# Performance work log

Measured on AMD Instinct MI355X. Metric: run time of the kernel, lower is better.

Reference implementation:

```python
import jax, jax.numpy as jnp
import numpy as np

LN_EPS = 1e-5

def _dw_conv_dilated(h, w, dil):
    # replicate-pad then VALID dilated depthwise 3x3 conv (groups = channels)
    hp = jnp.pad(h, ((0, 0), (0, 0), (dil, dil), (dil, dil)), mode='edge')
    return jax.lax.conv_general_dilated(
        hp, w, window_strides=(1, 1), padding='VALID', rhs_dilation=(dil, dil),
        dimension_numbers=('NCHW', 'OIHW', 'NCHW'), feature_group_count=h.shape[1])

def setup_inputs() -> dict:
    key = jax.random.key(0)
    ks = jax.random.split(key, 16)
    B, l, d_model = 4, 4096, 512
    d_inner, d_state, dt_rank = 512, 1, 32
    return {
        'x': jax.random.normal(ks[0], (B, l, d_model), jnp.float32),
        'in_proj_w': jax.random.normal(ks[1], (2 * d_inner, d_model), jnp.float32) * 0.02,
        'conv2d_w': jax.random.normal(ks[2], (d_inner, 1, 3, 3), jnp.float32) * 0.1,
        'conv2d_b': jax.random.normal(ks[3], (d_inner,), jnp.float32) * 0.1,
        'x_proj_weight': jax.random.normal(ks[4], (dt_rank + 2 * d_state, d_inner), jnp.float32) * 0.02,
        'dt_projs_weight': jax.random.normal(ks[5], (d_inner, dt_rank), jnp.float32) * 0.1,
        'dt_projs_bias': jax.random.normal(ks[6], (d_inner,), jnp.float32) * 0.1,
        'A_logs': jax.random.normal(ks[7], (d_inner, d_state), jnp.float32),
        'Ds': jax.random.normal(ks[8], (d_inner,), jnp.float32),
        'sf_k3': jax.random.normal(ks[9], (d_inner, 1, 3, 3), jnp.float32) * 0.1,
        'sf_k3_1': jax.random.normal(ks[10], (d_inner, 1, 3, 3), jnp.float32) * 0.1,
        'sf_k3_2': jax.random.normal(ks[11], (d_inner, 1, 3, 3), jnp.float32) * 0.1,
        'sf_alpha': jax.random.normal(ks[12], (3,), jnp.float32),
        'ln_w': jnp.ones((d_inner,), jnp.float32),
        'ln_b': jnp.zeros((d_inner,), jnp.float32),
        'out_proj_w': jax.random.normal(ks[13], (d_model, d_inner), jnp.float32) * 0.02,
    }

def reference(x, in_proj_w, conv2d_w, conv2d_b, x_proj_weight, dt_projs_weight,
              dt_projs_bias, A_logs, Ds, sf_k3, sf_k3_1, sf_k3_2, sf_alpha,
              ln_w, ln_b, out_proj_w):
    B, l, C = x.shape
    sqrt_l = int(np.ceil(np.sqrt(l)))
    new_l = sqrt_l * sqrt_l
    xp = jnp.pad(x, ((0, 0), (0, new_l - l), (0, 0)))
    xg = xp.reshape(B, sqrt_l, sqrt_l, C)                  # b h w c
    xz = xg @ in_proj_w.T                                  # b h w 2d
    d_inner = in_proj_w.shape[0] // 2
    xin, z = xz[..., :d_inner], xz[..., d_inner:]
    xc = jnp.transpose(xin, (0, 3, 1, 2))                  # b d h w
    xc = jax.lax.conv_general_dilated(
        xc, conv2d_w, (1, 1), 'SAME',
        dimension_numbers=('NCHW', 'OIHW', 'NCHW'),
        feature_group_count=d_inner) + conv2d_b[None, :, None, None]
    xc = jax.nn.silu(xc)
    H = W = sqrt_l
    L = H * W
    xs = xc.reshape(B, d_inner, L)                         # b d l
    x_dbl = jnp.einsum('kd,bdl->bkl', x_proj_weight, xs)
    R = dt_projs_weight.shape[1]
    N = A_logs.shape[1]                                    # == 1
    dts = jnp.einsum('dr,brl->bdl', dt_projs_weight, x_dbl[:, :R])
    Bs = x_dbl[:, R:R + N]                                 # b n l
    Cs = x_dbl[:, R + N:R + 2 * N]                         # b n l
    A = -jnp.exp(A_logs)                                   # d n
    delta = jax.nn.softplus(dts + dt_projs_bias[None, :, None])  # b d l
    # selective scan via associative scan: h_t = a_t * h_{t-1} + b_t
    a = jnp.exp(delta[:, :, None, :] * A[None, :, :, None])       # b d n l
    bb = delta[:, :, None, :] * Bs[:, None, :, :] * xs[:, :, None, :]
    def combine(c1, c2):
        a1, b1 = c1
        a2, b2 = c2
        return (a1 * a2, a2 * b1 + b2)
    _, h = jax.lax.associative_scan(combine, (a, bb), axis=-1)
    h = h[:, :, 0, :].reshape(B, d_inner, H, W)            # n == 1
    # StateFusion: 3 dilated replicate-padded depthwise convs
    h = (sf_alpha[0] * _dw_conv_dilated(h, sf_k3, 1)
         + sf_alpha[1] * _dw_conv_dilated(h, sf_k3_1, 2)
         + sf_alpha[2] * _dw_conv_dilated(h, sf_k3_2, 3))
    h = h.reshape(B, d_inner, L)
    y = h * Cs + xs * Ds[None, :, None]                    # Cs (b,1,l) broadcasts
    y = jnp.transpose(y, (0, 2, 1))                        # b l d
    mu = jnp.mean(y, axis=-1, keepdims=True)
    var = jnp.var(y, axis=-1, keepdims=True)
    y = (y - mu) / jnp.sqrt(var + LN_EPS) * ln_w + ln_b
    y = y * jax.nn.silu(z.reshape(B, L, d_inner))
    y = y @ out_proj_w.T
    return y[:, :l, :]
```

## Files before the change

kernel.cpp:

```cpp
#include <hip/hip_runtime.h>
#include <cstddef>


typedef __attribute__((ext_vector_type(8))) short short8;
typedef __attribute__((ext_vector_type(8))) unsigned short ushort8_t;
typedef __attribute__((ext_vector_type(4))) float f32x4;

__device__ __forceinline__ void gload16(const void* g, void* l) {
  __builtin_amdgcn_global_load_lds(
      (const __attribute__((address_space(1))) void*)g,
      (__attribute__((address_space(3))) void*)l, 16, 0, 0);
}

__device__ __forceinline__ void bf16split(float v, unsigned short& h, unsigned short& l) {
  unsigned u = __float_as_uint(v);
  unsigned uh = (u + 0x7fffu + ((u >> 16) & 1u)) & 0xffff0000u;
  h = (unsigned short)(uh >> 16);
  float rem = v - __uint_as_float(uh);
  unsigned ur = __float_as_uint(rem);
  l = (unsigned short)((ur + 0x7fffu + ((ur >> 16) & 1u)) >> 16);
}

__device__ __forceinline__ unsigned short bf16rne(float v) {
  unsigned u = __float_as_uint(v);
  return (unsigned short)((u + 0x7fffu + ((u >> 16) & 1u)) >> 16);
}

__device__ __forceinline__ float b2f(unsigned short u) {
  return __uint_as_float((unsigned)u << 16);
}

__global__ __launch_bounds__(256)
void split_k(const float* __restrict__ in, unsigned short* __restrict__ hi,
             unsigned short* __restrict__ lo, int n4)
{
  int i = blockIdx.x * 256 + threadIdx.x;
  if (i >= n4) return;
  float4 v = ((const float4*)in)[i];
  float vv[4] = {v.x, v.y, v.z, v.w};
  unsigned short h[4], l[4];
#pragma unroll
  for (int j = 0; j < 4; ++j) bf16split(vv[j], h[j], l[j]);
  ((ushort4*)hi)[i] = make_ushort4(h[0], h[1], h[2], h[3]);
  ((ushort4*)lo)[i] = make_ushort4(l[0], l[1], l[2], l[3]);
}

__global__ __launch_bounds__(256)
void cvt_hi_k(const float* __restrict__ in, unsigned short* __restrict__ hi, int n4)
{
  int i = blockIdx.x * 256 + threadIdx.x;
  if (i >= n4) return;
  float4 v = ((const float4*)in)[i];
  ((ushort4*)hi)[i] = make_ushort4(bf16rne(v.x), bf16rne(v.y), bf16rne(v.z), bf16rne(v.w));
}

__global__ __launch_bounds__(256, 2)
void gemm0_k(const unsigned short* __restrict__ Ahi, const unsigned short* __restrict__ Whi,
             const unsigned short* __restrict__ Wlo,
             unsigned short* __restrict__ xinb, unsigned short* __restrict__ zb16)
{
  __shared__ char smem[65536];
  unsigned short* sA  = (unsigned short*)smem;
  unsigned short* sBh = (unsigned short*)(smem + 32768);
  unsigned short* sBl = (unsigned short*)(smem + 49152);
  const int tid = threadIdx.x;
  const int wave = tid >> 6, lane = tid & 63;

  const int nwg = gridDim.x;
  const int q = nwg >> 3, r = nwg & 7;
  const int xcd = blockIdx.x & 7, wi = blockIdx.x >> 3;
  const int logical = (xcd < r ? xcd * (q + 1) : r * (q + 1) + (xcd - r) * q) + wi;
  const int tm = logical >> 3, tn = logical & 7;
  const int m0 = tm << 8;
  const int n0 = tn << 7;
  const bool two = (n0 < 512);

  const int wm = (wave & 1) << 7;
  const int wn = (wave >> 1) << 6;
  const int q16 = (lane >> 4) << 4;
  const int l15 = lane & 15;

  int srA[8], scA[8];
#pragma unroll
  for (int c = 0; c < 8; ++c) {
    int o = (wave << 13) + (c << 10) + (lane << 4);
    int row = o >> 7;
    srA[c] = row;
    scA[c] = (o & 127) ^ ((row & 7) << 4);
  }
  int srB[4], scB[4];
#pragma unroll
  for (int c = 0; c < 4; ++c) {
    int o = (wave << 12) + (c << 10) + (lane << 4);
    int row = o >> 7;
    srB[c] = row;
    scB[c] = (o & 127) ^ ((row & 7) << 4);
  }

  f32x4 acc[8][4];
#pragma unroll
  for (int i = 0; i < 8; ++i)
#pragma unroll
    for (int j = 0; j < 4; ++j) acc[i][j] = (f32x4){0.f, 0.f, 0.f, 0.f};

  for (int kt = 0; kt < 8; ++kt) {
    int kb = kt << 7;
    __syncthreads();
#pragma unroll
    for (int c = 0; c < 8; ++c)
      gload16((const char*)Ahi + (size_t)(m0 + srA[c]) * 1024 + kb + scA[c],
              (char*)sA + (wave << 13) + (c << 10));
#pragma unroll
    for (int c = 0; c < 4; ++c) {
      size_t gb = (size_t)(n0 + srB[c]) * 1024 + kb + scB[c];
      int lo_ = (wave << 12) + (c << 10);
      gload16((const char*)Whi + gb, (char*)sBh + lo_);
      if (two) gload16((const char*)Wlo + gb, (char*)sBl + lo_);
    }
    __syncthreads();
#pragma unroll
    for (int ks = 0; ks < 2; ++ks) {
      short8 af[8], bh[4], bl[4];
#pragma unroll
      for (int i = 0; i < 8; ++i) {
        int row = wm + (i << 4) + l15;
        int cb = ((ks << 6) + q16) ^ ((row & 7) << 4);
        af[i] = *(const short8*)((const char*)sA + (row << 7) + cb);
      }
#pragma unroll
      for (int j = 0; j < 4; ++j) {
        int row = wn + (j << 4) + l15;
        int cb = ((ks << 6) + q16) ^ ((row & 7) << 4);
        bh[j] = *(const short8*)((const char*)sBh + (row << 7) + cb);
        if (two) bl[j] = *(const short8*)((const char*)sBl + (row << 7) + cb);
      }
#pragma unroll
      for (int i = 0; i < 8; ++i)
#pragma unroll
        for (int j = 0; j < 4; ++j) {
          acc[i][j] = __builtin_amdgcn_mfma_f32_16x16x32_bf16(af[i], bh[j], acc[i][j], 0, 0, 0);
          if (two)
            acc[i][j] = __builtin_amdgcn_mfma_f32_16x16x32_bf16(af[i], bl[j], acc[i][j], 0, 0, 0);
        }
    }
  }

  const int mb_base = m0 + wm + ((lane >> 4) << 2);
#pragma unroll
  for (int j = 0; j < 4; ++j) {
    int n = n0 + wn + (j << 4) + l15;
#pragma unroll
    for (int i = 0; i < 8; ++i) {
      int mb = mb_base + (i << 4);
      if (n < 512) {
        int b = mb >> 12, l = mb & 4095;
        ushort4 hv = make_ushort4(bf16rne(acc[i][j][0]), bf16rne(acc[i][j][1]),
                                  bf16rne(acc[i][j][2]), bf16rne(acc[i][j][3]));
        *(ushort4*)&xinb[((size_t)(b * 512 + n) << 12) + l] = hv;
      } else {
#pragma unroll
        for (int rr = 0; rr < 4; ++rr)
          zb16[(size_t)(mb + rr) * 512 + (n - 512)] = bf16rne(acc[i][j][rr]);
      }
    }
  }
}

__global__ __launch_bounds__(256)
void gemm1_k(const unsigned short* __restrict__ Ag_, const unsigned short* __restrict__ Whi,
             float* __restrict__ o1)
{
  __shared__ char smem[32768];
  unsigned short* sA  = (unsigned short*)smem;
  unsigned short* sBh = (unsigned short*)(smem + 16384);
  const int tid = threadIdx.x;
  const int wave = tid >> 6, lane = tid & 63;

  const int nwg = gridDim.x;
  const int q = nwg >> 3, r = nwg & 7;
  const int xcd = blockIdx.x & 7, wi = blockIdx.x >> 3;
  const int logical = (xcd < r ? xcd * (q + 1) : r * (q + 1) + (xcd - r) * q) + wi;
  const int tm = logical >> 2, tn = logical & 3;
  const int m0 = tm << 7, n0 = tn << 7;

  const int wm = (wave & 1) << 6;
  const int wn = (wave >> 1) << 6;
  const int q16 = (lane >> 4) << 4;
  const int l15 = lane & 15;

  int srow[4], scol[4];
#pragma unroll
  for (int c = 0; c < 4; ++c) {
    int o = (wave << 12) + (c << 10) + (lane << 4);
    int row = o >> 7;
    srow[c] = row;
    scol[c] = (o & 127) ^ ((row & 7) << 4);
  }

  f32x4 acc[4][4];
#pragma unroll
  for (int i = 0; i < 4; ++i)
#pragma unroll
    for (int j = 0; j < 4; ++j) acc[i][j] = (f32x4){0.f, 0.f, 0.f, 0.f};

  for (int kt = 0; kt < 8; ++kt) {
    int kb = kt << 7;
    __syncthreads();
#pragma unroll
    for (int c = 0; c < 4; ++c) {
      size_t ga = (size_t)(m0 + srow[c]) * 1024 + kb + scol[c];
      size_t gb = (size_t)(n0 + srow[c]) * 1024 + kb + scol[c];
      int lo_ = (wave << 12) + (c << 10);
      gload16((const char*)Ag_ + ga, (char*)sA + lo_);
      gload16((const char*)Whi + gb, (char*)sBh + lo_);
    }
    __syncthreads();
#pragma unroll
    for (int ks = 0; ks < 2; ++ks) {
      short8 af[4], bh[4];
#pragma unroll
      for (int i = 0; i < 4; ++i) {
        int row = wm + (i << 4) + l15;
        int cb = ((ks << 6) + q16) ^ ((row & 7) << 4);
        af[i] = *(const short8*)((const char*)sA + (row << 7) + cb);
      }
#pragma unroll
      for (int j = 0; j < 4; ++j) {
        int row = wn + (j << 4) + l15;
        int cb = ((ks << 6) + q16) ^ ((row & 7) << 4);
        bh[j] = *(const short8*)((const char*)sBh + (row << 7) + cb);
      }
#pragma unroll
      for (int i = 0; i < 4; ++i)
#pragma unroll
        for (int j = 0; j < 4; ++j)
          acc[i][j] = __builtin_amdgcn_mfma_f32_16x16x32_bf16(af[i], bh[j], acc[i][j], 0, 0, 0);
    }
  }

  float* sC = (float*)smem;
  const int i_base = (lane >> 4) << 2;
#pragma unroll
  for (int half = 0; half < 2; ++half) {
    __syncthreads();
    if ((wave & 1) == half) {
#pragma unroll
      for (int j = 0; j < 4; ++j) {
        int nl = wn + (j << 4) + l15;
#pragma unroll
        for (int i = 0; i < 4; ++i) {
          int mloc = (i << 4) + i_base;
#pragma unroll
          for (int rr = 0; rr < 4; ++rr)
            sC[(mloc + rr) * 128 + nl] = acc[i][j][rr];
        }
      }
    }
    __syncthreads();
    int cx = (tid & 31) << 2;
    int r0 = tid >> 5;
#pragma unroll
    for (int it = 0; it < 8; ++it) {
      int row = r0 + (it << 3);
      *(float4*)&o1[(size_t)(m0 + (half << 6) + row) * 512 + n0 + cx] =
          *(float4*)&sC[row * 128 + cx];
    }
  }
}

__global__ __launch_bounds__(256)
void conv_silu_k(const unsigned short* __restrict__ xin, const float* __restrict__ w,
                 const float* __restrict__ bias, float* __restrict__ xs)
{
  __shared__ float t[64][65];
  int plane = blockIdx.x;
  int d = plane & 511;
  int tid = threadIdx.x;
  const unsigned short* src = xin + (size_t)plane * 4096;
  int l0 = tid << 4, row = tid >> 2, c0 = (tid & 3) << 4;
  ushort8_t v0 = *(const ushort8_t*)&src[l0];
  ushort8_t v1 = *(const ushort8_t*)&src[l0 + 8];
#pragma unroll
  for (int j = 0; j < 8; ++j) {
    t[row][c0 + j]     = b2f(v0[j]);
    t[row][c0 + 8 + j] = b2f(v1[j]);
  }
  float wv[9];
#pragma unroll
  for (int j = 0; j < 9; j++) wv[j] = w[d * 9 + j];
  float bv = bias[d];
  __syncthreads();
  float* dst = xs + (size_t)plane * 4096;
#pragma unroll
  for (int i = 0; i < 16; i++) {
    int idx = tid + i * 256;
    int y = idx >> 6, x = idx & 63;
    float s = bv;
#pragma unroll
    for (int u = 0; u < 3; u++)
#pragma unroll
      for (int v = 0; v < 3; v++) {
        int yy = y + u - 1, xx = x + v - 1;
        if (yy >= 0 && yy < 64 && xx >= 0 && xx < 64)
          s = fmaf(wv[u * 3 + v], t[yy][xx], s);
      }
    dst[idx] = s * (1.f / (1.f + __expf(-s)));
  }
}

__global__ __launch_bounds__(256)
void xdbl_part_k(const float* __restrict__ xs, const float* __restrict__ xpw,
                 float* __restrict__ partial)
{
  __shared__ float sw[34 * 64];
  int tid = threadIdx.x;
  int p  = blockIdx.x * 256 + tid;
  int d0 = blockIdx.y * 64;
  int b = p >> 12, l = p & 4095;
  for (int i = tid; i < 34 * 64; i += 256) {
    int k = i >> 6, dd = i & 63;
    sw[i] = xpw[k * 512 + d0 + dd];
  }
  __syncthreads();
  float acc[34];
#pragma unroll
  for (int k = 0; k < 34; k++) acc[k] = 0.f;
  const float* xp = xs + (size_t)(b * 512 + d0) * 4096 + l;
#pragma unroll 4
  for (int dd = 0; dd < 64; dd++) {
    float v = xp[(size_t)dd * 4096];
#pragma unroll
    for (int k = 0; k < 34; k++) acc[k] = fmaf(sw[k * 64 + dd], v, acc[k]);
  }
  float* op = partial + (size_t)blockIdx.y * 34 * 16384 + p;
#pragma unroll
  for (int k = 0; k < 34; k++) op[(size_t)k * 16384] = acc[k];
}

__global__ __launch_bounds__(256)
void xdbl_reduce_k(const float* __restrict__ partial, float* __restrict__ xdbl_r)
{
  int gid = blockIdx.x * 256 + threadIdx.x;
  float s = 0.f;
#pragma unroll
  for (int sp = 0; sp < 8; sp++) s += partial[(size_t)sp * 34 * 16384 + gid];
  xdbl_r[gid] = s;
}

__global__ __launch_bounds__(256)
void delta_k(const float* __restrict__ xdbl_r, const float* __restrict__ dtw,
             const float* __restrict__ dtb, float* __restrict__ del)
{
  __shared__ float sm[32][256];
  int tid = threadIdx.x;
  int l0 = blockIdx.x * 256;
  int d0 = blockIdx.y * 64;
  int b  = blockIdx.z;
  int p0 = b * 4096 + l0;
#pragma unroll
  for (int k = 0; k < 32; k++) sm[k][tid] = xdbl_r[k * 16384 + p0 + tid];
  __syncthreads();
#pragma unroll 2
  for (int dd = 0; dd < 64; dd++) {
    int d = d0 + dd;
    float s = dtb[d];
#pragma unroll
    for (int r = 0; r < 32; r++) s = fmaf(dtw[d * 32 + r], sm[r][tid], s);
    float delta = fmaxf(s, 0.f) + __logf(1.f + __expf(-fabsf(s)));
    del[((size_t)(b * 512 + d) << 12) + l0 + tid] = delta;
  }
}

__global__ __launch_bounds__(256)
void scan_sfconv_k(const float* __restrict__ del, const float* __restrict__ Bsr,
                   const float* __restrict__ xs, const float* __restrict__ A_logs,
                   const float* __restrict__ k1, const float* __restrict__ k2,
                   const float* __restrict__ k3, const float* __restrict__ alpha,
                   const float* __restrict__ Cs, const float* __restrict__ Ds,
                   unsigned short* __restrict__ ypre)
{
  __shared__ float t[64][65];
  __shared__ float segA[4], segH[4];
  int plane = blockIdx.x;
  int d = plane & 511;
  int b = plane >> 9;
  int tid = threadIdx.x;
  int wave = tid >> 6, lane = tid & 63;
  size_t base = (size_t)plane * 4096;
  float Ad = -__expf(A_logs[d]);

  const int l0 = tid << 4;
  float a_reg[16], b_reg[16], x_reg[16];
#pragma unroll
  for (int k = 0; k < 4; ++k) {
    float4 dv4 = *(const float4*)&del[base + l0 + k * 4];
    float4 bs4 = *(const float4*)&Bsr[(b << 12) + l0 + k * 4];
    float4 xs4 = *(const float4*)&xs[base + l0 + k * 4];
    float dv[4] = {dv4.x, dv4.y, dv4.z, dv4.w};
    float bs[4] = {bs4.x, bs4.y, bs4.z, bs4.w};
    float xv[4] = {xs4.x, xs4.y, xs4.z, xs4.w};
#pragma unroll
    for (int j = 0; j < 4; ++j) {
      a_reg[k * 4 + j] = __expf(dv[j] * Ad);
      b_reg[k * 4 + j] = dv[j] * bs[j] * xv[j];
      x_reg[k * 4 + j] = xv[j];
    }
  }

  float A_th = a_reg[0], H_th = b_reg[0];
#pragma unroll
  for (int j = 1; j < 16; ++j) {
    H_th = fmaf(a_reg[j], H_th, b_reg[j]);
    A_th *= a_reg[j];
  }

#pragma unroll
  for (int off = 1; off < 64; off <<= 1) {
    float Ap = __shfl_up(A_th, off);
    float Hp = __shfl_up(H_th, off);
    if (lane >= off) { H_th = fmaf(A_th, Hp, H_th); A_th *= Ap; }
  }
  float eA = __shfl_up(A_th, 1);
  float eH = __shfl_up(H_th, 1);
  if (lane == 0) { eA = 1.f; eH = 0.f; }
  if (lane == 63) { segA[wave] = A_th; segH[wave] = H_th; }
  __syncthreads();

  float cy1 = segH[0];
  float cy2 = fmaf(segA[1], cy1, segH[1]);
  float cy3 = fmaf(segA[2], cy2, segH[2]);
  float myc = (wave == 1) ? cy1 : (wave == 2) ? cy2 : (wave == 3) ? cy3 : 0.f;
  float h = fmaf(eA, myc, eH);

  int row = tid >> 2, c0 = (tid & 3) << 4;
#pragma unroll
  for (int j = 0; j < 16; ++j) {
    h = fmaf(a_reg[j], h, b_reg[j]);
    t[row][c0 + j] = h;
  }
  __syncthreads();

  float wv[3][9];
  float a0 = alpha[0], a1 = alpha[1], a2 = alpha[2];
#pragma unroll
  for (int j = 0; j < 9; j++) {
    wv[0][j] = a0 * k1[d * 9 + j];
    wv[1][j] = a1 * k2[d * 9 + j];
    wv[2][j] = a2 * k3[d * 9 + j];
  }
  float Dv = Ds[d];
  float cs_reg[16];
#pragma unroll
  for (int k = 0; k < 4; ++k) {
    float4 c4 = *(const float4*)&Cs[(b << 12) + l0 + k * 4];
    cs_reg[k * 4 + 0] = c4.x; cs_reg[k * 4 + 1] = c4.y;
    cs_reg[k * 4 + 2] = c4.z; cs_reg[k * 4 + 3] = c4.w;
  }
  unsigned short ov[16];
  const int y = row;
#pragma unroll
  for (int j = 0; j < 16; j++) {
    int x = c0 + j;
    float s = 0.f;
#pragma unroll
    for (int dil = 1; dil <= 3; dil++)
#pragma unroll
      for (int uu = 0; uu < 3; uu++)
#pragma unroll
        for (int vv = 0; vv < 3; vv++) {
          int yy = y + (uu - 1) * dil; yy = yy < 0 ? 0 : (yy > 63 ? 63 : yy);
          int xx = x + (vv - 1) * dil; xx = xx < 0 ? 0 : (xx > 63 ? 63 : xx);
          s = fmaf(wv[dil - 1][uu * 3 + vv], t[yy][xx], s);
        }
    ov[j] = bf16rne(fmaf(s, cs_reg[j], x_reg[j] * Dv));
  }
  ushort8_t o0, o1;
#pragma unroll
  for (int j = 0; j < 8; ++j) { o0[j] = ov[j]; o1[j] = ov[8 + j]; }
  *(ushort8_t*)&ypre[base + l0]     = o0;
  *(ushort8_t*)&ypre[base + l0 + 8] = o1;
}

__global__ __launch_bounds__(256)
void transpose_bf16_k(const unsigned short* __restrict__ src,
                      unsigned short* __restrict__ dst)
{
  __shared__ unsigned short t[64][72];
  int l0 = blockIdx.x * 64;
  int d0 = blockIdx.y * 64;
  int b  = blockIdx.z;
  int tid = threadIdx.x;
  int dl = tid & 63, lg0 = tid >> 6;
#pragma unroll
  for (int i = 0; i < 2; ++i) {
    int lg = lg0 + i * 4;
    ushort8_t v = *(const ushort8_t*)&src[(size_t)(b * 512 + d0 + dl) * 4096 + l0 + lg * 8];
#pragma unroll
    for (int j = 0; j < 8; ++j) t[lg * 8 + j][dl] = v[j];
  }
  __syncthreads();
  int pl = tid >> 2, c0 = (tid & 3) << 4;
  ushort8_t a = *(const ushort8_t*)&t[pl][c0];
  ushort8_t bb = *(const ushort8_t*)&t[pl][c0 + 8];
  size_t o = (size_t)(b * 4096 + l0 + pl) * 512 + d0 + c0;
  *(ushort8_t*)&dst[o] = a;
  *(ushort8_t*)&dst[o + 8] = bb;
}

__global__ __launch_bounds__(256)
void ln_silu_split_k(const unsigned short* __restrict__ y,
                     const unsigned short* __restrict__ z,
                     const float* __restrict__ lw, const float* __restrict__ lb,
                     unsigned short* __restrict__ hi)
{
  int wid = threadIdx.x >> 6, lane = threadIdx.x & 63;
  int pix = blockIdx.x * 4 + wid;
  const unsigned short* yp = y + (size_t)pix * 512;
  const unsigned short* zp = z + (size_t)pix * 512;
  ushort8_t yv8 = *(const ushort8_t*)&yp[lane * 8];
  float vv[8];
#pragma unroll
  for (int j = 0; j < 8; j++) vv[j] = b2f(yv8[j]);
  float sum = 0.f;
#pragma unroll
  for (int j = 0; j < 8; j++) sum += vv[j];
#pragma unroll
  for (int off = 1; off < 64; off <<= 1) sum += __shfl_xor(sum, off);
  float mu = sum * (1.f / 512.f);
  float q = 0.f;
#pragma unroll
  for (int j = 0; j < 8; j++) { float dd = vv[j] - mu; q += dd * dd; }
#pragma unroll
  for (int off = 1; off < 64; off <<= 1) q += __shfl_xor(q, off);
  float rstd = rsqrtf(q * (1.f / 512.f) + 1e-5f);
  ushort8_t zv8 = *(const ushort8_t*)&zp[lane * 8];
  unsigned short oh[8];
#pragma unroll
  for (int j = 0; j < 8; j++) {
    int dch = lane * 8 + j;
    float val = (vv[j] - mu) * rstd * lw[dch] + lb[dch];
    float zv = b2f(zv8[j]);
    float ov = val * (zv * (1.f / (1.f + __expf(-zv))));
    oh[j] = bf16rne(ov);
  }
  size_t o = (size_t)pix * 512 + lane * 8;
  *(ushort4*)&hi[o]     = make_ushort4(oh[0], oh[1], oh[2], oh[3]);
  *(ushort4*)&hi[o + 4] = make_ushort4(oh[4], oh[5], oh[6], oh[7]);
}

extern "C" void kernel_launch(void* const* d_in, const int* in_sizes, int n_in,
                              void* d_out, int out_size, void* d_ws, size_t ws_size,
                              hipStream_t stream)
{
  const float* x    = (const float*)d_in[0];
  const float* win  = (const float*)d_in[1];
  const float* cw   = (const float*)d_in[2];
  const float* cb   = (const float*)d_in[3];
  const float* xpw  = (const float*)d_in[4];
  const float* dtw  = (const float*)d_in[5];
  const float* dtb  = (const float*)d_in[6];
  const float* alog = (const float*)d_in[7];
  const float* Dsv  = (const float*)d_in[8];
  const float* k1   = (const float*)d_in[9];
  const float* k2   = (const float*)d_in[10];
  const float* k3   = (const float*)d_in[11];
  const float* alp  = (const float*)d_in[12];
  const float* lw   = (const float*)d_in[13];
  const float* lb   = (const float*)d_in[14];
  const float* wout = (const float*)d_in[15];
  float* out = (float*)d_out;

  const size_t NP = (size_t)4 * 512 * 4096;
  float* ws = (float*)d_ws;
  float* xs     = ws;
  float* zbuf   = ws + NP;
  float* w4     = ws + 2 * NP;
  float* xdbl_r = ws + 3 * NP;

  unsigned short* Ahi  = (unsigned short*)w4;
  unsigned short* Whi  = (unsigned short*)xs;
  unsigned short* Wlo  = Whi + (size_t)1024 * 512;
  unsigned short* xinb = (unsigned short*)d_out;
  unsigned short* zb16 = (unsigned short*)zbuf;
  unsigned short* yp16 = zb16 + (size_t)16384 * 512;
  unsigned short* yt16 = (unsigned short*)xs;
  unsigned short* Yhi  = (unsigned short*)w4;
  unsigned short* Ohi  = (unsigned short*)xs;
  float* xsf = xs;

  cvt_hi_k<<<8192, 256, 0, stream>>>(x, Ahi, 2097152);
  split_k<<<512, 256, 0, stream>>>(win, Whi, Wlo, 131072);
  gemm0_k<<<512, 256, 0, stream>>>(Ahi, Whi, Wlo, xinb, zb16);
  conv_silu_k<<<2048, 256, 0, stream>>>(xinb, cw, cb, xsf);
  xdbl_part_k<<<dim3(64, 8), 256, 0, stream>>>(xsf, xpw, out);
  xdbl_reduce_k<<<2176, 256, 0, stream>>>(out, xdbl_r);
  delta_k<<<dim3(16, 8, 4), 256, 0, stream>>>(xdbl_r, dtw, dtb, w4);
  scan_sfconv_k<<<2048, 256, 0, stream>>>(w4, xdbl_r + 32 * 16384, xsf, alog,
                                          k1, k2, k3, alp,
                                          xdbl_r + 33 * 16384, Dsv, yp16);
  transpose_bf16_k<<<dim3(64, 8, 4), 256, 0, stream>>>(yp16, yt16);
  ln_silu_split_k<<<4096, 256, 0, stream>>>(yt16, zb16, lw, lb, Yhi);
  cvt_hi_k<<<256, 256, 0, stream>>>(wout, Ohi, 65536);
  gemm1_k<<<512, 256, 0, stream>>>(Yhi, Ohi, out);
}
```

Baseline: 177.8 us.

## Double-buffer GEMM K-loops with smaller tiles and fuse input conversion kernels

Both bf16 GEMMs now use a 64-wide K step with two LDS buffers, so the global-to-LDS load of the next stage is issued while MFMAs run on the current one, and each iteration needs one barrier instead of two. gemm0 shrinks its M tile from 256 to 128, doubling the grid to 1024 blocks and cutting accumulator registers; it also drops the two-waves-per-SIMD launch bound. The x-to-bf16 conversion and the weight hi/lo split are merged into one launch. The trade-off is less data reuse per tile and more global loads per FLOP.

```diff
diff --git a/kernel.cpp b/kernel.cpp
--- a/kernel.cpp
+++ b/kernel.cpp
@@ -31,18 +31,25 @@
 }
 
 __global__ __launch_bounds__(256)
-void split_k(const float* __restrict__ in, unsigned short* __restrict__ hi,
-             unsigned short* __restrict__ lo, int n4)
-{
-  int i = blockIdx.x * 256 + threadIdx.x;
-  if (i >= n4) return;
-  float4 v = ((const float4*)in)[i];
-  float vv[4] = {v.x, v.y, v.z, v.w};
-  unsigned short h[4], l[4];
-#pragma unroll
-  for (int j = 0; j < 4; ++j) bf16split(vv[j], h[j], l[j]);
-  ((ushort4*)hi)[i] = make_ushort4(h[0], h[1], h[2], h[3]);
-  ((ushort4*)lo)[i] = make_ushort4(l[0], l[1], l[2], l[3]);
+void prep_k(const float* __restrict__ x, const float* __restrict__ win,
+            unsigned short* __restrict__ Ahi,
+            unsigned short* __restrict__ Whi, unsigned short* __restrict__ Wlo)
+{
+  int bid = blockIdx.x;
+  if (bid < 8192) {
+    int i = bid * 256 + threadIdx.x;
+    float4 v = ((const float4*)x)[i];
+    ((ushort4*)Ahi)[i] = make_ushort4(bf16rne(v.x), bf16rne(v.y), bf16rne(v.z), bf16rne(v.w));
+  } else {
+    int i = (bid - 8192) * 256 + threadIdx.x;
+    float4 v = ((const float4*)win)[i];
+    float vv[4] = {v.x, v.y, v.z, v.w};
+    unsigned short h[4], l[4];
+#pragma unroll
+    for (int j = 0; j < 4; ++j) bf16split(vv[j], h[j], l[j]);
+    ((ushort4*)Whi)[i] = make_ushort4(h[0], h[1], h[2], h[3]);
+    ((ushort4*)Wlo)[i] = make_ushort4(l[0], l[1], l[2], l[3]);
+  }
 }
 
 __global__ __launch_bounds__(256)
@@ -54,15 +61,12 @@
   ((ushort4*)hi)[i] = make_ushort4(bf16rne(v.x), bf16rne(v.y), bf16rne(v.z), bf16rne(v.w));
 }
 
-__global__ __launch_bounds__(256, 2)
+__global__ __launch_bounds__(256)
 void gemm0_k(const unsigned short* __restrict__ Ahi, const unsigned short* __restrict__ Whi,
              const unsigned short* __restrict__ Wlo,
              unsigned short* __restrict__ xinb, unsigned short* __restrict__ zb16)
 {
-  __shared__ char smem[65536];
-  unsigned short* sA  = (unsigned short*)smem;
-  unsigned short* sBh = (unsigned short*)(smem + 32768);
-  unsigned short* sBl = (unsigned short*)(smem + 49152);
+  __shared__ char smem[49152];
   const int tid = threadIdx.x;
   const int wave = tid >> 6, lane = tid & 63;
 
@@ -71,86 +75,85 @@
   const int xcd = blockIdx.x & 7, wi = blockIdx.x >> 3;
   const int logical = (xcd < r ? xcd * (q + 1) : r * (q + 1) + (xcd - r) * q) + wi;
   const int tm = logical >> 3, tn = logical & 7;
-  const int m0 = tm << 8;
-  const int n0 = tn << 7;
+  const int m0 = tm << 7, n0 = tn << 7;
   const bool two = (n0 < 512);
 
-  const int wm = (wave & 1) << 7;
+  const int wm = (wave & 1) << 6;
   const int wn = (wave >> 1) << 6;
   const int q16 = (lane >> 4) << 4;
   const int l15 = lane & 15;
 
-  int srA[8], scA[8];
-#pragma unroll
-  for (int c = 0; c < 8; ++c) {
-    int o = (wave << 13) + (c << 10) + (lane << 4);
-    int row = o >> 7;
-    srA[c] = row;
-    scA[c] = (o & 127) ^ ((row & 7) << 4);
-  }
-  int srB[4], scB[4];
-#pragma unroll
-  for (int c = 0; c < 4; ++c) {
-    int o = (wave << 12) + (c << 10) + (lane << 4);
-    int row = o >> 7;
-    srB[c] = row;
-    scB[c] = (o & 127) ^ ((row & 7) << 4);
-  }
-
-  f32x4 acc[8][4];
-#pragma unroll
-  for (int i = 0; i < 8; ++i)
+  int srow[2], scol[2];
+#pragma unroll
+  for (int c = 0; c < 2; ++c) {
+    int o = (wave << 11) + (c << 10) + (lane << 4);
+    int row = o >> 6;
+    srow[c] = row;
+    scol[c] = (o & 63) ^ ((row & 3) << 4);
+  }
+
+  f32x4 acc[4][4];
+#pragma unroll
+  for (int i = 0; i < 4; ++i)
 #pragma unroll
     for (int j = 0; j < 4; ++j) acc[i][j] = (f32x4){0.f, 0.f, 0.f, 0.f};
 
-  for (int kt = 0; kt < 8; ++kt) {
-    int kb = kt << 7;
+  const char* Ag = (const char*)Ahi;
+  const char* Bh = (const char*)Whi;
+  const char* Bl = (const char*)Wlo;
+
+#define G0_STAGE(buf, kt)                                                     \
+  {                                                                           \
+    char* base_ = smem + (buf) * 24576;                                       \
+    int kb_ = (kt) << 6;                                                      \
+    _Pragma("unroll")                                                         \
+    for (int c = 0; c < 2; ++c) {                                             \
+      int lo_ = (wave << 11) + (c << 10);                                     \
+      gload16(Ag + (size_t)(m0 + srow[c]) * 1024 + kb_ + scol[c], base_ + lo_);       \
+      gload16(Bh + (size_t)(n0 + srow[c]) * 1024 + kb_ + scol[c], base_ + 8192 + lo_);\
+      if (two)                                                                \
+        gload16(Bl + (size_t)(n0 + srow[c]) * 1024 + kb_ + scol[c], base_ + 16384 + lo_);\
+    }                                                                         \
+  }
+
+  G0_STAGE(0, 0);
+  __syncthreads();
+  for (int kt = 0; kt < 16; ++kt) {
+    int cur = kt & 1;
+    if (kt < 15) G0_STAGE(cur ^ 1, kt + 1);
+    const char* bp = smem + cur * 24576;
+    short8 af[4], bh[4], bl[4];
+#pragma unroll
+    for (int i = 0; i < 4; ++i) {
+      int row = wm + (i << 4) + l15;
+      int cb = q16 ^ ((row & 3) << 4);
+      af[i] = *(const short8*)(bp + (row << 6) + cb);
+    }
+#pragma unroll
+    for (int j = 0; j < 4; ++j) {
+      int row = wn + (j << 4) + l15;
+      int cb = q16 ^ ((row & 3) << 4);
+      bh[j] = *(const short8*)(bp + 8192 + (row << 6) + cb);
+      if (two) bl[j] = *(const short8*)(bp + 16384 + (row << 6) + cb);
+    }
+#pragma unroll
+    for (int i = 0; i < 4; ++i)
+#pragma unroll
+      for (int j = 0; j < 4; ++j) {
+        acc[i][j] = __builtin_amdgcn_mfma_f32_16x16x32_bf16(af[i], bh[j], acc[i][j], 0, 0, 0);
+        if (two)
+          acc[i][j] = __builtin_amdgcn_mfma_f32_16x16x32_bf16(af[i], bl[j], acc[i][j], 0, 0, 0);
+      }
     __syncthreads();
-#pragma unroll
-    for (int c = 0; c < 8; ++c)
-      gload16((const char*)Ahi + (size_t)(m0 + srA[c]) * 1024 + kb + scA[c],
-              (char*)sA + (wave << 13) + (c << 10));
-#pragma unroll
-    for (int c = 0; c < 4; ++c) {
-      size_t gb = (size_t)(n0 + srB[c]) * 1024 + kb + scB[c];
-      int lo_ = (wave << 12) + (c << 10);
-      gload16((const char*)Whi + gb, (char*)sBh + lo_);
-      if (two) gload16((const char*)Wlo + gb, (char*)sBl + lo_);
-    }
-    __syncthreads();
-#pragma unroll
-    for (int ks = 0; ks < 2; ++ks) {
-      short8 af[8], bh[4], bl[4];
-#pragma unroll
-      for (int i = 0; i < 8; ++i) {
-        int row = wm + (i << 4) + l15;
-        int cb = ((ks << 6) + q16) ^ ((row & 7) << 4);
-        af[i] = *(const short8*)((const char*)sA + (row << 7) + cb);
-      }
-#pragma unroll
-      for (int j = 0; j < 4; ++j) {
-        int row = wn + (j << 4) + l15;
-        int cb = ((ks << 6) + q16) ^ ((row & 7) << 4);
-        bh[j] = *(const short8*)((const char*)sBh + (row << 7) + cb);
-        if (two) bl[j] = *(const short8*)((const char*)sBl + (row << 7) + cb);
-      }
-#pragma unroll
-      for (int i = 0; i < 8; ++i)
-#pragma unroll
-        for (int j = 0; j < 4; ++j) {
-          acc[i][j] = __builtin_amdgcn_mfma_f32_16x16x32_bf16(af[i], bh[j], acc[i][j], 0, 0, 0);
-          if (two)
-            acc[i][j] = __builtin_amdgcn_mfma_f32_16x16x32_bf16(af[i], bl[j], acc[i][j], 0, 0, 0);
-        }
-    }
-  }
+  }
+#undef G0_STAGE
 
   const int mb_base = m0 + wm + ((lane >> 4) << 2);
 #pragma unroll
   for (int j = 0; j < 4; ++j) {
     int n = n0 + wn + (j << 4) + l15;
 #pragma unroll
-    for (int i = 0; i < 8; ++i) {
+    for (int i = 0; i < 4; ++i) {
       int mb = mb_base + (i << 4);
       if (n < 512) {
         int b = mb >> 12, l = mb & 4095;
@@ -171,8 +174,6 @@
              float* __restrict__ o1)
 {
   __shared__ char smem[32768];
-  unsigned short* sA  = (unsigned short*)smem;
-  unsigned short* sBh = (unsigned short*)(smem + 16384);
   const int tid = threadIdx.x;
   const int wave = tid >> 6, lane = tid & 63;
 
@@ -188,13 +189,13 @@
   const int q16 = (lane >> 4) << 4;
   const int l15 = lane & 15;
 
-  int srow[4], scol[4];
-#pragma unroll
-  for (int c = 0; c < 4; ++c) {
-    int o = (wave << 12) + (c << 10) + (lane << 4);
-    int row = o >> 7;
+  int srow[2], scol[2];
+#pragma unroll
+  for (int c = 0; c < 2; ++c) {
+    int o = (wave << 11) + (c << 10) + (lane << 4);
+    int row = o >> 6;
     srow[c] = row;
-    scol[c] = (o & 127) ^ ((row & 7) << 4);
+    scol[c] = (o & 63) ^ ((row & 3) << 4);
   }
 
   f32x4 acc[4][4];
@@ -203,40 +204,48 @@
 #pragma unroll
     for (int j = 0; j < 4; ++j) acc[i][j] = (f32x4){0.f, 0.f, 0.f, 0.f};
 
-  for (int kt = 0; kt < 8; ++kt) {
-    int kb = kt << 7;
+  const char* Ag = (const char*)Ag_;
+  const char* Bg = (const char*)Whi;
+
+#define G1_STAGE(buf, kt)                                                     \
+  {                                                                           \
+    char* base_ = smem + (buf) * 16384;                                       \
+    int kb_ = (kt) << 6;                                                      \
+    _Pragma("unroll")                                                         \
+    for (int c = 0; c < 2; ++c) {                                             \
+      int lo_ = (wave << 11) + (c << 10);                                     \
+      gload16(Ag + (size_t)(m0 + srow[c]) * 1024 + kb_ + scol[c], base_ + lo_);       \
+      gload16(Bg + (size_t)(n0 + srow[c]) * 1024 + kb_ + scol[c], base_ + 8192 + lo_);\
+    }                                                                         \
+  }
+
+  G1_STAGE(0, 0);
+  __syncthreads();
+  for (int kt = 0; kt < 16; ++kt) {
+    int cur = kt & 1;
+    if (kt < 15) G1_STAGE(cur ^ 1, kt + 1);
+    const char* bp = smem + cur * 16384;
+    short8 af[4], bh[4];
+#pragma unroll
+    for (int i = 0; i < 4; ++i) {
+      int row = wm + (i << 4) + l15;
+      int cb = q16 ^ ((row & 3) << 4);
+      af[i] = *(const short8*)(bp + (row << 6) + cb);
+    }
+#pragma unroll
+    for (int j = 0; j < 4; ++j) {
+      int row = wn + (j << 4) + l15;
+      int cb = q16 ^ ((row & 3) << 4);
+      bh[j] = *(const short8*)(bp + 8192 + (row << 6) + cb);
+    }
+#pragma unroll
+    for (int i = 0; i < 4; ++i)
+#pragma unroll
+      for (int j = 0; j < 4; ++j)
+        acc[i][j] = __builtin_amdgcn_mfma_f32_16x16x32_bf16(af[i], bh[j], acc[i][j], 0, 0, 0);
     __syncthreads();
-#pragma unroll
-    for (int c = 0; c < 4; ++c) {
-      size_t ga = (size_t)(m0 + srow[c]) * 1024 + kb + scol[c];
-      size_t gb = (size_t)(n0 + srow[c]) * 1024 + kb + scol[c];
-      int lo_ = (wave << 12) + (c << 10);
-      gload16((const char*)Ag_ + ga, (char*)sA + lo_);
-      gload16((const char*)Whi + gb, (char*)sBh + lo_);
-    }
-    __syncthreads();
-#pragma unroll
-    for (int ks = 0; ks < 2; ++ks) {
-      short8 af[4], bh[4];
-#pragma unroll
-      for (int i = 0; i < 4; ++i) {
-        int row = wm + (i << 4) + l15;
-        int cb = ((ks << 6) + q16) ^ ((row & 7) << 4);
-        af[i] = *(const short8*)((const char*)sA + (row << 7) + cb);
-      }
-#pragma unroll
-      for (int j = 0; j < 4; ++j) {
-        int row = wn + (j << 4) + l15;
-        int cb = ((ks << 6) + q16) ^ ((row & 7) << 4);
-        bh[j] = *(const short8*)((const char*)sBh + (row << 7) + cb);
-      }
-#pragma unroll
-      for (int i = 0; i < 4; ++i)
-#pragma unroll
-        for (int j = 0; j < 4; ++j)
-          acc[i][j] = __builtin_amdgcn_mfma_f32_16x16x32_bf16(af[i], bh[j], acc[i][j], 0, 0, 0);
-    }
-  }
+  }
+#undef G1_STAGE
 
   float* sC = (float*)smem;
   const int i_base = (lane >> 4) << 2;
@@ -588,9 +597,8 @@
   unsigned short* Ohi  = (unsigned short*)xs;
   float* xsf = xs;
 
-  cvt_hi_k<<<8192, 256, 0, stream>>>(x, Ahi, 2097152);
-  split_k<<<512, 256, 0, stream>>>(win, Whi, Wlo, 131072);
-  gemm0_k<<<512, 256, 0, stream>>>(Ahi, Whi, Wlo, xinb, zb16);
+  prep_k<<<8704, 256, 0, stream>>>(x, win, Ahi, Whi, Wlo);
+  gemm0_k<<<1024, 256, 0, stream>>>(Ahi, Whi, Wlo, xinb, zb16);
   conv_silu_k<<<2048, 256, 0, stream>>>(xinb, cw, cb, xsf);
   xdbl_part_k<<<dim3(64, 8), 256, 0, stream>>>(xsf, xpw, out);
   xdbl_reduce_k<<<2176, 256, 0, stream>>>(out, xdbl_r);
```

Result: no change. 177.4 us (-0.2%).
